# Kernel tuning notes

Hardware: AMD Instinct MI355X
Metric: run time of the kernel (lower is better)

The kernel has to match this reference:

```python
import jax, jax.numpy as jnp
import numpy as np

VOCAB, EMB, HID, OUT = 32000, 512, 1024, 8
B, S = 128, 512


def setup_inputs() -> dict:
    key = jax.random.key(0)
    ks = jax.random.split(key, 7)
    sequence_ids = jax.random.randint(ks[0], (B, S), 0, VOCAB)
    scale = 0.02
    emb = jax.random.normal(ks[1], (VOCAB, EMB), dtype=jnp.float32) * scale
    W_ih = jax.random.normal(ks[2], (4 * HID, EMB), dtype=jnp.float32) * scale
    W_hh = jax.random.normal(ks[3], (4 * HID, HID), dtype=jnp.float32) * scale
    b = jax.random.normal(ks[4], (4 * HID,), dtype=jnp.float32) * scale
    W_out = jax.random.normal(ks[5], (OUT, HID), dtype=jnp.float32) * scale
    b_out = jax.random.normal(ks[6], (OUT,), dtype=jnp.float32) * scale
    return {"sequence_ids": sequence_ids, "emb": emb, "W_ih": W_ih, "W_hh": W_hh,
            "b": b, "W_out": W_out, "b_out": b_out}


def reference(sequence_ids, emb, W_ih, W_hh, b, W_out, b_out):
    # embedding lookup: [B, S, E]
    x = emb[sequence_ids]
    Bb = x.shape[0]
    H = W_hh.shape[1]
    # precompute input projections for all timesteps at once: [S, B, 4H]
    xg = jnp.einsum('bse,ge->sbg', x, W_ih) + b

    def step(carry, xg_t):
        h, c = carry
        gates = xg_t + h @ W_hh.T  # [B, 4H]
        i, f, g, o = jnp.split(gates, 4, axis=-1)
        c = jax.nn.sigmoid(f) * c + jax.nn.sigmoid(i) * jnp.tanh(g)
        h = jax.nn.sigmoid(o) * jnp.tanh(c)
        return (h, c), None

    h0 = jnp.zeros((Bb, H), x.dtype)
    (h_last, _), _ = jax.lax.scan(step, (h0, h0), xg)
    # classifier on last hidden state: [B, OUT]
    return h_last @ W_out.T + b_out
```

## Files before the change

### kernel.cpp

```cpp
#include <hip/hip_runtime.h>
#include <cstdint>
#include <cstddef>

#define SEQ    512
#define BATCH  128
#define EMB    512
#define HID    1024
#define KTOT   1536
#define NOUT   8

#define RG     4
#define NBQ    64
#define NBLK   (RG*NBQ)
#define ROWS   32

typedef unsigned short u16;
typedef unsigned int   u32;
typedef unsigned long long u64;
typedef __attribute__((ext_vector_type(8))) __bf16 bf16x8;
typedef __attribute__((ext_vector_type(4))) float  f32x4;
typedef __attribute__((ext_vector_type(4))) float  float4v;
typedef __attribute__((ext_vector_type(4))) u16    u16x4;

#define OFF_X    0ull
#define SZ_X     ((size_t)SEQ*BATCH*EMB*2)
#define OFF_W    (OFF_X + SZ_X)
#define SZ_W     ((size_t)4*HID*KTOT*2)
#define OFF_RING (OFF_W + SZ_W)
#define SZ_RING  ((size_t)(SEQ+1)*BATCH*HID*2)
#define OFF_CNT  (OFF_RING + SZ_RING)
#define SZ_CNT   ((size_t)16*RG*64)
#define OFF_GO   (OFF_CNT + SZ_CNT)
#define SZ_GO    ((size_t)RG*64)
#define WS_NEED  (OFF_GO + SZ_GO)

__device__ inline u16 f2b(float f) {
  uint32_t u = __builtin_bit_cast(uint32_t, f);
  u = u + 0x7FFFu + ((u >> 16) & 1u);
  return (u16)(u >> 16);
}
__device__ inline float b2f(u16 u) {
  uint32_t v = ((uint32_t)u) << 16;
  return __builtin_bit_cast(float, v);
}
__device__ inline float sigm(float x) { return 1.0f / (1.0f + __expf(-x)); }
__device__ inline float tanh_(float x) {
  x = fminf(fmaxf(x, -15.f), 15.f);
  float e = __expf(2.f * x);
  return (e - 1.f) / (e + 1.f);
}
__device__ inline f32x4 mfma16(bf16x8 a, bf16x8 b, f32x4 c) {
  return __builtin_amdgcn_mfma_f32_16x16x32_bf16(a, b, c, 0, 0, 0);
}

__global__ void embed_kernel(const int* __restrict__ ids,
                             const float* __restrict__ emb,
                             u16* __restrict__ x) {
  int bid = blockIdx.x;
  int t = bid >> 7, b = bid & 127;
  int idx = ids[b * SEQ + t];
  const float4v* src = (const float4v*)(emb + (size_t)idx * EMB);
  float4v v = src[threadIdx.x];
  u16x4 o;
  o.x = f2b(v.x); o.y = f2b(v.y); o.z = f2b(v.z); o.w = f2b(v.w);
  *(u16x4*)(x + (size_t)bid * EMB + threadIdx.x * 4) = o;
}

__global__ void wpack_kernel(const float* __restrict__ Wih,
                             const float* __restrict__ Whh,
                             u16* __restrict__ Wp) {
  int gc = blockIdx.x;
  int unit = gc >> 2, q = gc & 3;
  int row = q * HID + unit;
  u16* dst = Wp + (size_t)gc * KTOT;
  for (int k = threadIdx.x; k < KTOT; k += 256) {
    float v = (k < EMB) ? Wih[(size_t)row * EMB + k]
                        : Whh[(size_t)row * HID + (k - EMB)];
    dst[k] = f2b(v);
  }
}

__global__ __launch_bounds__(256, 1) void lstm_kernel(
    const u16* __restrict__ x,
    const u16* __restrict__ Wp,
    const float* __restrict__ bias,
    u16* __restrict__ ring,
    u32* __restrict__ cnt,
    u32* __restrict__ go)
{
  __shared__ float pacc[4][ROWS][68];

  const int tid  = threadIdx.x;
  const int bid  = blockIdx.x;
  const int rg   = bid & 3;
  const int nb   = bid >> 2;
  const int lane = tid & 63;
  const int kq   = tid >> 6;
  const int l15  = lane & 15;
  const int lhi  = lane >> 4;

  const int nxc  = (kq == 0) ? 12 : (kq == 1 ? 4 : 0);
  const int arow = rg * ROWS + l15;

  bf16x8 wreg[12][4];
  {
    const int colbase = nb * 64;
    #pragma unroll
    for (int c = 0; c < 12; ++c)
      #pragma unroll
      for (int nt = 0; nt < 4; ++nt)
        wreg[c][nt] = *(const bf16x8*)(Wp
            + (size_t)(colbase + nt * 16 + l15) * KTOT
            + kq * 384 + c * 32 + lhi * 8);
  }

  const int urow = tid >> 3;
  const int up   = tid & 7;
  const int rowg = rg * ROWS + urow;
  float bs[2][4];
  #pragma unroll
  for (int k = 0; k < 2; ++k) {
    int ug = nb * 16 + 2 * up + k;
    #pragma unroll
    for (int q = 0; q < 4; ++q) bs[k][q] = bias[q * HID + ug];
  }
  float cst[2] = {0.f, 0.f};

  u32* gol = &go[rg * 16];

  bf16x8 af[2][12];
  #pragma unroll
  for (int c = 0; c < 12; ++c)
    if (c < nxc) {
      #pragma unroll
      for (int mt = 0; mt < 2; ++mt)
        af[mt][c] = *(const bf16x8*)(x + (size_t)(arow + mt * 16) * EMB
                                     + kq * 384 + c * 32 + lhi * 8);
    }

  #pragma unroll 1
  for (int t = 0; t < SEQ; ++t) {
    f32x4 acc[2][4];
    #pragma unroll
    for (int mt = 0; mt < 2; ++mt)
      #pragma unroll
      for (int nt = 0; nt < 4; ++nt) acc[mt][nt] = (f32x4){0.f, 0.f, 0.f, 0.f};
    #pragma unroll
    for (int c = 0; c < 12; ++c)
      if (c < nxc) {
        #pragma unroll
        for (int mt = 0; mt < 2; ++mt)
          #pragma unroll
          for (int nt = 0; nt < 4; ++nt)
            acc[mt][nt] = mfma16(af[mt][c], wreg[c][nt], acc[mt][nt]);
      }

    if (t > 0) {
      if (tid == 0) {
        while (__hip_atomic_load(gol, __ATOMIC_RELAXED,
                                 __HIP_MEMORY_SCOPE_AGENT) < (u32)t)
          __builtin_amdgcn_s_sleep(1);
        __asm__ __volatile__("" ::: "memory");
      }
      __syncthreads();
    }

    {
      const u16* hb = ring + (size_t)t * (BATCH * HID);
      #pragma unroll
      for (int c = 0; c < 12; ++c)
        if (c >= nxc) {
          #pragma unroll
          for (int mt = 0; mt < 2; ++mt)
            af[mt][c] = *(const bf16x8*)(hb + (size_t)(arow + mt * 16) * HID
                                         + (kq * 384 - 512 + c * 32) + lhi * 8);
        }
    }

    {
      int tn = (t + 1 < SEQ) ? (t + 1) : t;
      const u16* xb = x + (size_t)tn * (BATCH * EMB);
      #pragma unroll
      for (int c = 0; c < 12; ++c)
        if (c < nxc) {
          #pragma unroll
          for (int mt = 0; mt < 2; ++mt)
            af[mt][c] = *(const bf16x8*)(xb + (size_t)(arow + mt * 16) * EMB
                                         + kq * 384 + c * 32 + lhi * 8);
        }
    }

    #pragma unroll
    for (int c = 0; c < 12; ++c)
      if (c >= nxc) {
        #pragma unroll
        for (int mt = 0; mt < 2; ++mt)
          #pragma unroll
          for (int nt = 0; nt < 4; ++nt)
            acc[mt][nt] = mfma16(af[mt][c], wreg[c][nt], acc[mt][nt]);
      }

    #pragma unroll
    for (int mt = 0; mt < 2; ++mt)
      #pragma unroll
      for (int nt = 0; nt < 4; ++nt)
        #pragma unroll
        for (int rr = 0; rr < 4; ++rr) {
          int row = mt * 16 + lhi * 4 + rr;
          int c   = nt * 16 + l15;
          int pc  = (c & ~7) | ((c ^ row) & 7);
          pacc[kq][row][pc] = acc[mt][nt][rr];
        }
    __syncthreads();

    {
      float s[2][4];
      #pragma unroll
      for (int k = 0; k < 2; ++k)
        #pragma unroll
        for (int q = 0; q < 4; ++q) s[k][q] = bs[k][q];
      #pragma unroll
      for (int k2 = 0; k2 < 4; ++k2)
        #pragma unroll
        for (int cl = 0; cl < 8; ++cl) {
          int pc = 8 * up + ((cl ^ urow) & 7);
          s[cl >> 2][cl & 3] += pacc[k2][urow][pc];
        }
      float hv2[2];
      #pragma unroll
      for (int k = 0; k < 2; ++k) {
        float cn = sigm(s[k][1]) * cst[k] + sigm(s[k][0]) * tanh_(s[k][2]);
        cst[k] = cn;
        hv2[k] = sigm(s[k][3]) * tanh_(cn);
      }
      u32 val = (u32)f2b(hv2[0]) | ((u32)f2b(hv2[1]) << 16);
      u32* dst = (u32*)(ring + (size_t)(t + 1) * (BATCH * HID)
                        + (size_t)rowg * HID + nb * 16 + 2 * up);
      asm volatile("global_store_dword %0, %1, off sc0 sc1"
                   :: "v"(dst), "v"(val) : "memory");
    }
    asm volatile("s_waitcnt vmcnt(0)" ::: "memory");

    __syncthreads();
    if (t == SEQ - 1) break;
    if (tid == 0) {
      u32* cl_ = &cnt[((size_t)(t & 15) * RG + rg) * 16];
      u32 old = __hip_atomic_fetch_add(cl_, 1u, __ATOMIC_RELAXED,
                                       __HIP_MEMORY_SCOPE_AGENT);
      if (old == (u32)(NBQ - 1)) {
        __hip_atomic_store(cl_, 0u, __ATOMIC_RELAXED,
                           __HIP_MEMORY_SCOPE_AGENT);
        __hip_atomic_store(gol, (u32)(t + 1), __ATOMIC_RELAXED,
                           __HIP_MEMORY_SCOPE_AGENT);
      }
    }
  }
}

__global__ void head_kernel(const u16* __restrict__ h,
                            const float* __restrict__ Wout,
                            const float* __restrict__ bout,
                            float* __restrict__ out) {
  int b = blockIdx.x, l = threadIdx.x;
  float p[NOUT];
  #pragma unroll
  for (int o = 0; o < NOUT; ++o) p[o] = 0.f;
  for (int k = l; k < HID; k += 64) {
    float hv = b2f(h[(size_t)b * HID + k]);
    #pragma unroll
    for (int o = 0; o < NOUT; ++o) p[o] += hv * Wout[(size_t)o * HID + k];
  }
  #pragma unroll
  for (int o = 0; o < NOUT; ++o) {
    float v = p[o];
    #pragma unroll
    for (int off = 32; off > 0; off >>= 1) v += __shfl_down(v, off);
    if (l == 0) out[b * NOUT + o] = v + bout[o];
  }
}

__global__ void sentinel_kernel(float* out, int n) {
  int i = blockIdx.x * 256 + threadIdx.x;
  if (i < n) out[i] = 1e9f;
}

extern "C" void kernel_launch(void* const* d_in, const int* in_sizes, int n_in,
                              void* d_out, int out_size, void* d_ws, size_t ws_size,
                              hipStream_t stream) {
  const int*   ids  = (const int*)d_in[0];
  const float* emb  = (const float*)d_in[1];
  const float* Wih  = (const float*)d_in[2];
  const float* Whh  = (const float*)d_in[3];
  const float* bias = (const float*)d_in[4];
  const float* Wout = (const float*)d_in[5];
  const float* bout = (const float*)d_in[6];
  float* out = (float*)d_out;

  if (ws_size < WS_NEED) {
    sentinel_kernel<<<(out_size + 255) / 256, 256, 0, stream>>>(out, out_size);
    return;
  }

  char* ws = (char*)d_ws;
  u16* x    = (u16*)(ws + OFF_X);
  u16* Wp   = (u16*)(ws + OFF_W);
  u16* ring = (u16*)(ws + OFF_RING);
  u32* cnt  = (u32*)(ws + OFF_CNT);
  u32* go   = (u32*)(ws + OFF_GO);

  hipMemsetAsync(ring, 0, (size_t)BATCH * HID * 2, stream);
  hipMemsetAsync(cnt, 0, SZ_CNT + SZ_GO, stream);

  embed_kernel<<<SEQ * BATCH, 128, 0, stream>>>(ids, emb, x);
  wpack_kernel<<<4 * HID, 256, 0, stream>>>(Wih, Whh, Wp);

  lstm_kernel<<<NBLK, 256, 0, stream>>>(x, Wp, bias, ring, cnt, go);

  head_kernel<<<BATCH, 64, 0, stream>>>(ring + (size_t)SEQ * BATCH * HID,
                                        Wout, bout, out);
}
```

Baseline: 3.176 ms.

## Split per-row-group barrier into per-K-slice sub-barriers with per-wave waits

Replaces the single per-row-group global flag with three sub-group flags, one for each slice of hidden units that a K-quarter wave consumes. Each wave polls only the flag for its own slice, and each wave's lane 0 signals arrival, so waves can start on the slices that are ready instead of waiting for all 64 blocks. The goal is to shorten the critical path of the per-timestep global barrier. In exchange it adds more atomic traffic, drops the block-wide syncthreads around the wait, and uses a bail-out counter that could silently skip synchronization.

Result: slower. 3.302 ms (+4.0%).

```diff
diff --git a/kernel.cpp b/kernel.cpp
--- a/kernel.cpp
+++ b/kernel.cpp
@@ -13,6 +13,7 @@
 #define NBQ    64
 #define NBLK   (RG*NBQ)
 #define ROWS   32
+#define NSG    3
 
 typedef unsigned short u16;
 typedef unsigned int   u32;
@@ -29,10 +30,10 @@
 #define OFF_RING (OFF_W + SZ_W)
 #define SZ_RING  ((size_t)(SEQ+1)*BATCH*HID*2)
 #define OFF_CNT  (OFF_RING + SZ_RING)
-#define SZ_CNT   ((size_t)16*RG*64)
-#define OFF_GO   (OFF_CNT + SZ_CNT)
-#define SZ_GO    ((size_t)RG*64)
-#define WS_NEED  (OFF_GO + SZ_GO)
+#define SZ_CNT   ((size_t)16*RG*NSG*64)
+#define OFF_SGO  (OFF_CNT + SZ_CNT)
+#define SZ_SGO   ((size_t)RG*NSG*64)
+#define WS_NEED  (OFF_SGO + SZ_SGO)
 
 __device__ inline u16 f2b(float f) {
   uint32_t u = __builtin_bit_cast(uint32_t, f);
@@ -86,7 +87,7 @@
     const float* __restrict__ bias,
     u16* __restrict__ ring,
     u32* __restrict__ cnt,
-    u32* __restrict__ go)
+    u32* __restrict__ subgo)
 {
   __shared__ float pacc[4][ROWS][68];
 
@@ -102,6 +103,12 @@
   const int nxc  = (kq == 0) ? 12 : (kq == 1 ? 4 : 0);
   const int arow = rg * ROWS + l15;
 
+  const int grp  = (nb < 16) ? 0 : (nb < 40 ? 1 : 2);
+  const u32 agt  = (grp == 0) ? 64u : 96u;
+  u32* sgo_pub  = &subgo[((size_t)rg * NSG + grp) * 16];
+  const u32* sgo_mine = (kq > 0)
+      ? &subgo[((size_t)rg * NSG + (kq - 1)) * 16] : nullptr;
+
   bf16x8 wreg[12][4];
   {
     const int colbase = nb * 64;
@@ -126,8 +133,6 @@
   }
   float cst[2] = {0.f, 0.f};
 
-  u32* gol = &go[rg * 16];
-
   bf16x8 af[2][12];
   #pragma unroll
   for (int c = 0; c < 12; ++c)
@@ -155,14 +160,17 @@
             acc[mt][nt] = mfma16(af[mt][c], wreg[c][nt], acc[mt][nt]);
       }
 
-    if (t > 0) {
-      if (tid == 0) {
-        while (__hip_atomic_load(gol, __ATOMIC_RELAXED,
-                                 __HIP_MEMORY_SCOPE_AGENT) < (u32)t)
-          __builtin_amdgcn_s_sleep(1);
-        __asm__ __volatile__("" ::: "memory");
-      }
-      __syncthreads();
+    if (t > 0 && kq > 0) {
+      const u32 tgt = (u32)t;
+      int bail = 0;
+      for (;;) {
+        u32 v = __hip_atomic_load(sgo_mine, __ATOMIC_RELAXED,
+                                  __HIP_MEMORY_SCOPE_AGENT);
+        if (__all(v >= tgt)) break;
+        if (++bail > (1 << 20)) break;
+        __builtin_amdgcn_s_sleep(1);
+      }
+      __asm__ __volatile__("" ::: "memory");
     }
 
     {
@@ -213,19 +221,20 @@
         }
     __syncthreads();
 
+    float s[2][4];
+    #pragma unroll
+    for (int k = 0; k < 2; ++k)
+      #pragma unroll
+      for (int q = 0; q < 4; ++q) s[k][q] = bs[k][q];
+    #pragma unroll
+    for (int k2 = 0; k2 < 4; ++k2)
+      #pragma unroll
+      for (int cl = 0; cl < 8; ++cl) {
+        int pc = 8 * up + ((cl ^ urow) & 7);
+        s[cl >> 2][cl & 3] += pacc[k2][urow][pc];
+      }
+    __syncthreads();
     {
-      float s[2][4];
-      #pragma unroll
-      for (int k = 0; k < 2; ++k)
-        #pragma unroll
-        for (int q = 0; q < 4; ++q) s[k][q] = bs[k][q];
-      #pragma unroll
-      for (int k2 = 0; k2 < 4; ++k2)
-        #pragma unroll
-        for (int cl = 0; cl < 8; ++cl) {
-          int pc = 8 * up + ((cl ^ urow) & 7);
-          s[cl >> 2][cl & 3] += pacc[k2][urow][pc];
-        }
       float hv2[2];
       #pragma unroll
       for (int k = 0; k < 2; ++k) {
@@ -241,17 +250,17 @@
     }
     asm volatile("s_waitcnt vmcnt(0)" ::: "memory");
 
-    __syncthreads();
-    if (t == SEQ - 1) break;
-    if (tid == 0) {
-      u32* cl_ = &cnt[((size_t)(t & 15) * RG + rg) * 16];
-      u32 old = __hip_atomic_fetch_add(cl_, 1u, __ATOMIC_RELAXED,
-                                       __HIP_MEMORY_SCOPE_AGENT);
-      if (old == (u32)(NBQ - 1)) {
-        __hip_atomic_store(cl_, 0u, __ATOMIC_RELAXED,
-                           __HIP_MEMORY_SCOPE_AGENT);
-        __hip_atomic_store(gol, (u32)(t + 1), __ATOMIC_RELAXED,
-                           __HIP_MEMORY_SCOPE_AGENT);
+    if (t < SEQ - 1) {
+      if (lane == 0) {
+        u32* cl_ = &cnt[((((size_t)(t & 15) * RG) + rg) * NSG + grp) * 16];
+        u32 old = __hip_atomic_fetch_add(cl_, 1u, __ATOMIC_RELAXED,
+                                         __HIP_MEMORY_SCOPE_AGENT);
+        if (old == agt - 1u) {
+          __hip_atomic_store(cl_, 0u, __ATOMIC_RELAXED,
+                             __HIP_MEMORY_SCOPE_AGENT);
+          __hip_atomic_store(sgo_pub, (u32)(t + 1), __ATOMIC_RELAXED,
+                             __HIP_MEMORY_SCOPE_AGENT);
+        }
       }
     }
   }
@@ -302,19 +311,19 @@
   }
 
   char* ws = (char*)d_ws;
-  u16* x    = (u16*)(ws + OFF_X);
-  u16* Wp   = (u16*)(ws + OFF_W);
-  u16* ring = (u16*)(ws + OFF_RING);
-  u32* cnt  = (u32*)(ws + OFF_CNT);
-  u32* go   = (u32*)(ws + OFF_GO);
+  u16* x     = (u16*)(ws + OFF_X);
+  u16* Wp    = (u16*)(ws + OFF_W);
+  u16* ring  = (u16*)(ws + OFF_RING);
+  u32* cnt   = (u32*)(ws + OFF_CNT);
+  u32* subgo = (u32*)(ws + OFF_SGO);
 
   hipMemsetAsync(ring, 0, (size_t)BATCH * HID * 2, stream);
-  hipMemsetAsync(cnt, 0, SZ_CNT + SZ_GO, stream);
+  hipMemsetAsync(cnt, 0, SZ_CNT + SZ_SGO, stream);
 
   embed_kernel<<<SEQ * BATCH, 128, 0, stream>>>(ids, emb, x);
   wpack_kernel<<<4 * HID, 256, 0, stream>>>(Wih, Whh, Wp);
 
-  lstm_kernel<<<NBLK, 256, 0, stream>>>(x, Wp, bias, ring, cnt, go);
+  lstm_kernel<<<NBLK, 256, 0, stream>>>(x, Wp, bias, ring, cnt, subgo);
 
   head_kernel<<<BATCH, 64, 0, stream>>>(ring + (size_t)SEQ * BATCH * HID,
                                         Wout, bout, out);
```

## Replace per-group barrier counter with per-wave flags and fine-grained dependency polling

Applied to the files above, without the earlier changes.

Swaps the global atomic counter plus single go-flag barrier for per-wave progress flags. Each wave that consumes recurrent h state polls only the flags of the producer blocks whose h columns it reads, using lane-parallel loads combined with a wave vote. The x-only wave no longer waits at all. This removes the serialized atomic fetch-add, the trailing block barrier and the tid0 spin, at the cost of more polling traffic and a bail-out limit that could let a wave proceed with stale data.

After: 3.073 ms. -3.2%, faster.

```diff
diff --git a/kernel.cpp b/kernel.cpp
--- a/kernel.cpp
+++ b/kernel.cpp
@@ -28,11 +28,9 @@
 #define SZ_W     ((size_t)4*HID*KTOT*2)
 #define OFF_RING (OFF_W + SZ_W)
 #define SZ_RING  ((size_t)(SEQ+1)*BATCH*HID*2)
-#define OFF_CNT  (OFF_RING + SZ_RING)
-#define SZ_CNT   ((size_t)16*RG*64)
-#define OFF_GO   (OFF_CNT + SZ_CNT)
-#define SZ_GO    ((size_t)RG*64)
-#define WS_NEED  (OFF_GO + SZ_GO)
+#define OFF_FW   (OFF_RING + SZ_RING)
+#define SZ_FW    ((size_t)RG*NBQ*4*64)
+#define WS_NEED  (OFF_FW + SZ_FW)
 
 __device__ inline u16 f2b(float f) {
   uint32_t u = __builtin_bit_cast(uint32_t, f);
@@ -85,8 +83,7 @@
     const u16* __restrict__ Wp,
     const float* __restrict__ bias,
     u16* __restrict__ ring,
-    u32* __restrict__ cnt,
-    u32* __restrict__ go)
+    u32* __restrict__ fw)
 {
   __shared__ float pacc[4][ROWS][68];
 
@@ -102,6 +99,15 @@
   const int nxc  = (kq == 0) ? 12 : (kq == 1 ? 4 : 0);
   const int arow = rg * ROWS + l15;
 
+  u32* fw_own = &fw[(((size_t)rg * NBQ + nb) * 4 + kq) * 16];
+  const int pbase = (kq == 1) ? 0 : (kq == 2 ? 16 : 40);
+  const int nflag = (kq == 1) ? 64 : 96;
+  const u32* fp0 = &fw[(((size_t)rg * NBQ + pbase + (lane >> 2)) * 4 + (lane & 3)) * 16];
+  const int  f2i = lane + 64;
+  const u32* fp1 = (f2i < nflag)
+      ? &fw[(((size_t)rg * NBQ + pbase + (f2i >> 2)) * 4 + (f2i & 3)) * 16]
+      : fp0;
+
   bf16x8 wreg[12][4];
   {
     const int colbase = nb * 64;
@@ -126,8 +132,6 @@
   }
   float cst[2] = {0.f, 0.f};
 
-  u32* gol = &go[rg * 16];
-
   bf16x8 af[2][12];
   #pragma unroll
   for (int c = 0; c < 12; ++c)
@@ -155,14 +159,17 @@
             acc[mt][nt] = mfma16(af[mt][c], wreg[c][nt], acc[mt][nt]);
       }
 
-    if (t > 0) {
-      if (tid == 0) {
-        while (__hip_atomic_load(gol, __ATOMIC_RELAXED,
-                                 __HIP_MEMORY_SCOPE_AGENT) < (u32)t)
-          __builtin_amdgcn_s_sleep(1);
-        __asm__ __volatile__("" ::: "memory");
-      }
-      __syncthreads();
+    if (t > 0 && kq > 0) {
+      const u32 tgt = (u32)t;
+      int bail = 0;
+      for (;;) {
+        u32 a = __hip_atomic_load(fp0, __ATOMIC_RELAXED, __HIP_MEMORY_SCOPE_AGENT);
+        u32 b = __hip_atomic_load(fp1, __ATOMIC_RELAXED, __HIP_MEMORY_SCOPE_AGENT);
+        if (__all((a >= tgt) & (b >= tgt))) break;
+        if (++bail > (1 << 20)) break;
+        __builtin_amdgcn_s_sleep(1);
+      }
+      __asm__ __volatile__("" ::: "memory");
     }
 
     {
@@ -213,19 +220,21 @@
         }
     __syncthreads();
 
+    float s[2][4];
+    #pragma unroll
+    for (int k = 0; k < 2; ++k)
+      #pragma unroll
+      for (int q = 0; q < 4; ++q) s[k][q] = bs[k][q];
+    #pragma unroll
+    for (int k2 = 0; k2 < 4; ++k2)
+      #pragma unroll
+      for (int cl = 0; cl < 8; ++cl) {
+        int pc = 8 * up + ((cl ^ urow) & 7);
+        s[cl >> 2][cl & 3] += pacc[k2][urow][pc];
+      }
+    __syncthreads();
+
     {
-      float s[2][4];
-      #pragma unroll
-      for (int k = 0; k < 2; ++k)
-        #pragma unroll
-        for (int q = 0; q < 4; ++q) s[k][q] = bs[k][q];
-      #pragma unroll
-      for (int k2 = 0; k2 < 4; ++k2)
-        #pragma unroll
-        for (int cl = 0; cl < 8; ++cl) {
-          int pc = 8 * up + ((cl ^ urow) & 7);
-          s[cl >> 2][cl & 3] += pacc[k2][urow][pc];
-        }
       float hv2[2];
       #pragma unroll
       for (int k = 0; k < 2; ++k) {
@@ -241,18 +250,9 @@
     }
     asm volatile("s_waitcnt vmcnt(0)" ::: "memory");
 
-    __syncthreads();
-    if (t == SEQ - 1) break;
-    if (tid == 0) {
-      u32* cl_ = &cnt[((size_t)(t & 15) * RG + rg) * 16];
-      u32 old = __hip_atomic_fetch_add(cl_, 1u, __ATOMIC_RELAXED,
-                                       __HIP_MEMORY_SCOPE_AGENT);
-      if (old == (u32)(NBQ - 1)) {
-        __hip_atomic_store(cl_, 0u, __ATOMIC_RELAXED,
-                           __HIP_MEMORY_SCOPE_AGENT);
-        __hip_atomic_store(gol, (u32)(t + 1), __ATOMIC_RELAXED,
-                           __HIP_MEMORY_SCOPE_AGENT);
-      }
+    if (t < SEQ - 1 && lane == 0) {
+      __hip_atomic_store(fw_own, (u32)(t + 1), __ATOMIC_RELAXED,
+                         __HIP_MEMORY_SCOPE_AGENT);
     }
   }
 }
@@ -305,16 +305,15 @@
   u16* x    = (u16*)(ws + OFF_X);
   u16* Wp   = (u16*)(ws + OFF_W);
   u16* ring = (u16*)(ws + OFF_RING);
-  u32* cnt  = (u32*)(ws + OFF_CNT);
-  u32* go   = (u32*)(ws + OFF_GO);
+  u32* fwv  = (u32*)(ws + OFF_FW);
 
   hipMemsetAsync(ring, 0, (size_t)BATCH * HID * 2, stream);
-  hipMemsetAsync(cnt, 0, SZ_CNT + SZ_GO, stream);
+  hipMemsetAsync(fwv, 0, SZ_FW, stream);
 
   embed_kernel<<<SEQ * BATCH, 128, 0, stream>>>(ids, emb, x);
   wpack_kernel<<<4 * HID, 256, 0, stream>>>(Wih, Whh, Wp);
 
-  lstm_kernel<<<NBLK, 256, 0, stream>>>(x, Wp, bias, ring, cnt, go);
+  lstm_kernel<<<NBLK, 256, 0, stream>>>(x, Wp, bias, ring, fwv);
 
   head_kernel<<<BATCH, 64, 0, stream>>>(ring + (size_t)SEQ * BATCH * HID,
                                         Wout, bout, out);
```

## Repartition LSTM into 8 batch pods with per-block flags and XCC-local sync

Applied to the files above, without the earlier changes.

Repartitions the persistent LSTM grid into 8 batch pods of 16 rows by 32 column blocks, each holding 128 gate columns. 96 columns live in registers and 32 in LDS. The central counter-plus-go barrier is replaced by per-block progress flags that 32 lanes poll in parallel. Each block records its XCC ID at startup, and when all blocks in a pod share one XCC it uses non-coherent-scope stores and loads to cut cross-die cache traffic. The risks are extra LDS weight reads inside the inner MFMA loop, and a correctness dependence on how the hardware places blocks onto XCCs.

Result: slower. 3.392 ms (+6.8%).

```diff
diff --git a/kernel.cpp b/kernel.cpp
--- a/kernel.cpp
+++ b/kernel.cpp
@@ -9,14 +9,16 @@
 #define KTOT   1536
 #define NOUT   8
 
-#define RG     4
-#define NBQ    64
-#define NBLK   (RG*NBQ)
-#define ROWS   32
+#define NPOD   8
+#define NCB    32
+#define NBLK   (NPOD*NCB)
+#define ROWS   16
+#define WLSTR  1544
+
+#define GETREG_XCC 63508
 
 typedef unsigned short u16;
 typedef unsigned int   u32;
-typedef unsigned long long u64;
 typedef __attribute__((ext_vector_type(8))) __bf16 bf16x8;
 typedef __attribute__((ext_vector_type(4))) float  f32x4;
 typedef __attribute__((ext_vector_type(4))) float  float4v;
@@ -28,11 +30,15 @@
 #define SZ_W     ((size_t)4*HID*KTOT*2)
 #define OFF_RING (OFF_W + SZ_W)
 #define SZ_RING  ((size_t)(SEQ+1)*BATCH*HID*2)
-#define OFF_CNT  (OFF_RING + SZ_RING)
-#define SZ_CNT   ((size_t)16*RG*64)
-#define OFF_GO   (OFF_CNT + SZ_CNT)
-#define SZ_GO    ((size_t)RG*64)
-#define WS_NEED  (OFF_GO + SZ_GO)
+#define OFF_FW   (OFF_RING + SZ_RING)
+#define SZ_FW    ((size_t)NBLK*64)
+#define OFF_XT   (OFF_FW + SZ_FW)
+#define SZ_XT    (4096ull)
+#define WS_NEED  (OFF_XT + SZ_XT)
+
+#define SMEM_W   ((size_t)32*WLSTR*2)
+#define SMEM_P   ((size_t)4*ROWS*136*4)
+#define SMEM_BYTES (SMEM_W + SMEM_P)
 
 __device__ inline u16 f2b(float f) {
   uint32_t u = __builtin_bit_cast(uint32_t, f);
@@ -85,81 +91,129 @@
     const u16* __restrict__ Wp,
     const float* __restrict__ bias,
     u16* __restrict__ ring,
-    u32* __restrict__ cnt,
-    u32* __restrict__ go)
+    u32* __restrict__ fw,
+    u32* __restrict__ xtab)
 {
-  __shared__ float pacc[4][ROWS][68];
+  extern __shared__ char smem[];
+  u16*   wl   = (u16*)smem;
+  float* pacc = (float*)(smem + SMEM_W);
+  __shared__ int smode;
 
   const int tid  = threadIdx.x;
   const int bid  = blockIdx.x;
-  const int rg   = bid & 3;
-  const int nb   = bid >> 2;
+  const int pod  = bid & 7;
+  const int cb   = bid >> 3;
   const int lane = tid & 63;
   const int kq   = tid >> 6;
   const int l15  = lane & 15;
   const int lhi  = lane >> 4;
 
   const int nxc  = (kq == 0) ? 12 : (kq == 1 ? 4 : 0);
-  const int arow = rg * ROWS + l15;
-
-  bf16x8 wreg[12][4];
+  const int arow = pod * ROWS + l15;
+
+  const u32 myx = (__builtin_amdgcn_s_getreg(GETREG_XCC) & 0xFu) | 0x10u;
+  if (tid == 0) {
+    smode = 0;
+    __hip_atomic_store(&xtab[bid], myx, __ATOMIC_RELAXED,
+                       __HIP_MEMORY_SCOPE_AGENT);
+  }
+
+  bf16x8 wreg[12][6];
   {
-    const int colbase = nb * 64;
+    const int colbase = cb * 128;
     #pragma unroll
     for (int c = 0; c < 12; ++c)
       #pragma unroll
-      for (int nt = 0; nt < 4; ++nt)
+      for (int nt = 0; nt < 6; ++nt)
         wreg[c][nt] = *(const bf16x8*)(Wp
             + (size_t)(colbase + nt * 16 + l15) * KTOT
             + kq * 384 + c * 32 + lhi * 8);
   }
-
-  const int urow = tid >> 3;
-  const int up   = tid & 7;
-  const int rowg = rg * ROWS + urow;
+  for (int e = tid * 8; e < 32 * KTOT; e += 256 * 8) {
+    int col = e / KTOT;
+    int k   = e - col * KTOT;
+    *(bf16x8*)&wl[col * WLSTR + k] =
+        *(const bf16x8*)(Wp + (size_t)(cb * 128 + 96 + col) * KTOT + k);
+  }
+
+  __syncthreads();
+  if (tid < 64) {
+    const int peer = 8 * (lane & 31) + pod;
+    u32 xv = 0; int bail = 0;
+    for (;;) {
+      xv = __hip_atomic_load(&xtab[peer], __ATOMIC_RELAXED,
+                             __HIP_MEMORY_SCOPE_AGENT);
+      if (xv != 0) break;
+      if (++bail > (1 << 18)) break;
+      __builtin_amdgcn_s_sleep(1);
+    }
+    int ok = __all(xv == myx) ? 1 : 0;
+    if (lane == 0) smode = ok;
+  }
+  __syncthreads();
+  const int fast = smode;
+
+  const int urow = tid >> 4;
+  const int u    = tid & 15;
   float bs[2][4];
   #pragma unroll
   for (int k = 0; k < 2; ++k) {
-    int ug = nb * 16 + 2 * up + k;
+    int ug = cb * 32 + u + k * 16;
     #pragma unroll
     for (int q = 0; q < 4; ++q) bs[k][q] = bias[q * HID + ug];
   }
   float cst[2] = {0.f, 0.f};
 
-  u32* gol = &go[rg * 16];
-
-  bf16x8 af[2][12];
+  const u16* wlb  = &wl[l15 * WLSTR + kq * 384 + lhi * 8];
+  u32* fw_own = &fw[(size_t)bid * 16];
+
+  bf16x8 af[12];
   #pragma unroll
   for (int c = 0; c < 12; ++c)
-    if (c < nxc) {
-      #pragma unroll
-      for (int mt = 0; mt < 2; ++mt)
-        af[mt][c] = *(const bf16x8*)(x + (size_t)(arow + mt * 16) * EMB
-                                     + kq * 384 + c * 32 + lhi * 8);
-    }
+    if (c < nxc)
+      af[c] = *(const bf16x8*)(x + (size_t)arow * EMB + kq * 384 + c * 32 + lhi * 8);
 
   #pragma unroll 1
   for (int t = 0; t < SEQ; ++t) {
-    f32x4 acc[2][4];
-    #pragma unroll
-    for (int mt = 0; mt < 2; ++mt)
-      #pragma unroll
-      for (int nt = 0; nt < 4; ++nt) acc[mt][nt] = (f32x4){0.f, 0.f, 0.f, 0.f};
+    f32x4 acc[8];
+    #pragma unroll
+    for (int nt = 0; nt < 8; ++nt) acc[nt] = (f32x4){0.f, 0.f, 0.f, 0.f};
     #pragma unroll
     for (int c = 0; c < 12; ++c)
       if (c < nxc) {
         #pragma unroll
-        for (int mt = 0; mt < 2; ++mt)
-          #pragma unroll
-          for (int nt = 0; nt < 4; ++nt)
-            acc[mt][nt] = mfma16(af[mt][c], wreg[c][nt], acc[mt][nt]);
+        for (int nt = 0; nt < 6; ++nt)
+          acc[nt] = mfma16(af[c], wreg[c][nt], acc[nt]);
+        bf16x8 w6 = *(const bf16x8*)(wlb + c * 32);
+        bf16x8 w7 = *(const bf16x8*)(wlb + 16 * WLSTR + c * 32);
+        acc[6] = mfma16(af[c], w6, acc[6]);
+        acc[7] = mfma16(af[c], w7, acc[7]);
       }
 
     if (t > 0) {
-      if (tid == 0) {
-        while (__hip_atomic_load(gol, __ATOMIC_RELAXED,
-                                 __HIP_MEMORY_SCOPE_AGENT) < (u32)t)
-          __builtin_amdgcn_s_sleep(1);
+      if (tid < 64) {
+        const u32 tgt = (u32)t;
+        const u32* fp = &fw[(size_t)(8 * (lane & 31) + pod) * 16];
+        int bail = 0;
+        if (fast) {
+          for (;;) {
+            u32 v;
+            asm volatile("global_load_dword %0, %1, off sc0\n\t"
+                         "s_waitcnt vmcnt(0)"
+                         : "=v"(v) : "v"(fp) : "memory");
+            if (__all(v >= tgt)) break;
+            if (++bail > (1 << 18)) break;
+            __builtin_amdgcn_s_sleep(1);
+          }
+        } else {
+          for (;;) {
+            u32 v = __hip_atomic_load(fp, __ATOMIC_RELAXED,
+                                      __HIP_MEMORY_SCOPE_AGENT);
+            if (__all(v >= tgt)) break;
+            if (++bail > (1 << 18)) break;
+            __builtin_amdgcn_s_sleep(1);
+          }
+        }
         __asm__ __volatile__("" ::: "memory");
       }
       __syncthreads();
@@ -169,12 +223,9 @@
       const u16* hb = ring + (size_t)t * (BATCH * HID);
       #pragma unroll
       for (int c = 0; c < 12; ++c)
-        if (c >= nxc) {
-          #pragma unroll
-          for (int mt = 0; mt < 2; ++mt)
-            af[mt][c] = *(const bf16x8*)(hb + (size_t)(arow + mt * 16) * HID
-                                         + (kq * 384 - 512 + c * 32) + lhi * 8);
-        }
+        if (c >= nxc)
+          af[c] = *(const bf16x8*)(hb + (size_t)arow * HID
+                                   + (kq * 384 - 512 + c * 32) + lhi * 8);
     }
 
     {
@@ -182,50 +233,52 @@
       const u16* xb = x + (size_t)tn * (BATCH * EMB);
       #pragma unroll
       for (int c = 0; c < 12; ++c)
-        if (c < nxc) {
-          #pragma unroll
-          for (int mt = 0; mt < 2; ++mt)
-            af[mt][c] = *(const bf16x8*)(xb + (size_t)(arow + mt * 16) * EMB
-                                         + kq * 384 + c * 32 + lhi * 8);
-        }
+        if (c < nxc)
+          af[c] = *(const bf16x8*)(xb + (size_t)arow * EMB
+                                   + kq * 384 + c * 32 + lhi * 8);
     }
 
     #pragma unroll
     for (int c = 0; c < 12; ++c)
       if (c >= nxc) {
         #pragma unroll
-        for (int mt = 0; mt < 2; ++mt)
-          #pragma unroll
-          for (int nt = 0; nt < 4; ++nt)
-            acc[mt][nt] = mfma16(af[mt][c], wreg[c][nt], acc[mt][nt]);
-      }
-
-    #pragma unroll
-    for (int mt = 0; mt < 2; ++mt)
-      #pragma unroll
-      for (int nt = 0; nt < 4; ++nt)
+        for (int nt = 0; nt < 6; ++nt)
+          acc[nt] = mfma16(af[c], wreg[c][nt], acc[nt]);
+        bf16x8 w6 = *(const bf16x8*)(wlb + c * 32);
+        bf16x8 w7 = *(const bf16x8*)(wlb + 16 * WLSTR + c * 32);
+        acc[6] = mfma16(af[c], w6, acc[6]);
+        acc[7] = mfma16(af[c], w7, acc[7]);
+      }
+
+    #pragma unroll
+    for (int nt = 0; nt < 8; ++nt)
+      #pragma unroll
+      for (int rr = 0; rr < 4; ++rr) {
+        int row = lhi * 4 + rr;
+        int c   = nt * 16 + l15;
+        int pc  = (c & ~7) | ((c ^ row) & 7);
+        pacc[(kq * ROWS + row) * 136 + pc] = acc[nt][rr];
+      }
+    __syncthreads();
+
+    float s[2][4];
+    #pragma unroll
+    for (int k = 0; k < 2; ++k)
+      #pragma unroll
+      for (int q = 0; q < 4; ++q) s[k][q] = bs[k][q];
+    #pragma unroll
+    for (int k2 = 0; k2 < 4; ++k2)
+      #pragma unroll
+      for (int k = 0; k < 2; ++k)
         #pragma unroll
-        for (int rr = 0; rr < 4; ++rr) {
-          int row = mt * 16 + lhi * 4 + rr;
-          int c   = nt * 16 + l15;
-          int pc  = (c & ~7) | ((c ^ row) & 7);
-          pacc[kq][row][pc] = acc[mt][nt][rr];
+        for (int q = 0; q < 4; ++q) {
+          int c  = (u + k * 16) * 4 + q;
+          int pc = (c & ~7) | ((c ^ urow) & 7);
+          s[k][q] += pacc[(k2 * ROWS + urow) * 136 + pc];
         }
     __syncthreads();
 
     {
-      float s[2][4];
-      #pragma unroll
-      for (int k = 0; k < 2; ++k)
-        #pragma unroll
-        for (int q = 0; q < 4; ++q) s[k][q] = bs[k][q];
-      #pragma unroll
-      for (int k2 = 0; k2 < 4; ++k2)
-        #pragma unroll
-        for (int cl = 0; cl < 8; ++cl) {
-          int pc = 8 * up + ((cl ^ urow) & 7);
-          s[cl >> 2][cl & 3] += pacc[k2][urow][pc];
-        }
       float hv2[2];
       #pragma unroll
       for (int k = 0; k < 2; ++k) {
@@ -233,24 +286,37 @@
         cst[k] = cn;
         hv2[k] = sigm(s[k][3]) * tanh_(cn);
       }
-      u32 val = (u32)f2b(hv2[0]) | ((u32)f2b(hv2[1]) << 16);
-      u32* dst = (u32*)(ring + (size_t)(t + 1) * (BATCH * HID)
-                        + (size_t)rowg * HID + nb * 16 + 2 * up);
-      asm volatile("global_store_dword %0, %1, off sc0 sc1"
-                   :: "v"(dst), "v"(val) : "memory");
+      float o0 = __shfl_xor(hv2[0], 1);
+      float o1 = __shfl_xor(hv2[1], 1);
+      if ((u & 1) == 0) {
+        u16* hw = ring + (size_t)(t + 1) * (BATCH * HID)
+                  + (size_t)(pod * ROWS + urow) * HID + cb * 32;
+        u32 v0 = (u32)f2b(hv2[0]) | ((u32)f2b(o0) << 16);
+        u32 v1 = (u32)f2b(hv2[1]) | ((u32)f2b(o1) << 16);
+        u32* d0 = (u32*)&hw[u];
+        u32* d1 = (u32*)&hw[u + 16];
+        if (fast) {
+          asm volatile("global_store_dword %0, %2, off\n\t"
+                       "global_store_dword %1, %3, off"
+                       :: "v"(d0), "v"(d1), "v"(v0), "v"(v1) : "memory");
+        } else {
+          asm volatile("global_store_dword %0, %2, off sc0 sc1\n\t"
+                       "global_store_dword %1, %3, off sc0 sc1"
+                       :: "v"(d0), "v"(d1), "v"(v0), "v"(v1) : "memory");
+        }
+      }
     }
     asm volatile("s_waitcnt vmcnt(0)" ::: "memory");
 
     __syncthreads();
     if (t == SEQ - 1) break;
     if (tid == 0) {
-      u32* cl_ = &cnt[((size_t)(t & 15) * RG + rg) * 16];
-      u32 old = __hip_atomic_fetch_add(cl_, 1u, __ATOMIC_RELAXED,
-                                       __HIP_MEMORY_SCOPE_AGENT);
-      if (old == (u32)(NBQ - 1)) {
-        __hip_atomic_store(cl_, 0u, __ATOMIC_RELAXED,
-                           __HIP_MEMORY_SCOPE_AGENT);
-        __hip_atomic_store(gol, (u32)(t + 1), __ATOMIC_RELAXED,
+      u32 v = (u32)(t + 1);
+      if (fast) {
+        asm volatile("global_store_dword %0, %1, off sc0"
+                     :: "v"(fw_own), "v"(v) : "memory");
+      } else {
+        __hip_atomic_store(fw_own, v, __ATOMIC_RELAXED,
                            __HIP_MEMORY_SCOPE_AGENT);
       }
     }
@@ -305,16 +371,19 @@
   u16* x    = (u16*)(ws + OFF_X);
   u16* Wp   = (u16*)(ws + OFF_W);
   u16* ring = (u16*)(ws + OFF_RING);
-  u32* cnt  = (u32*)(ws + OFF_CNT);
-  u32* go   = (u32*)(ws + OFF_GO);
+  u32* fwv  = (u32*)(ws + OFF_FW);
+  u32* xtab = (u32*)(ws + OFF_XT);
 
   hipMemsetAsync(ring, 0, (size_t)BATCH * HID * 2, stream);
-  hipMemsetAsync(cnt, 0, SZ_CNT + SZ_GO, stream);
+  hipMemsetAsync(fwv, 0, SZ_FW + SZ_XT, stream);
 
   embed_kernel<<<SEQ * BATCH, 128, 0, stream>>>(ids, emb, x);
   wpack_kernel<<<4 * HID, 256, 0, stream>>>(Wih, Whh, Wp);
 
-  lstm_kernel<<<NBLK, 256, 0, stream>>>(x, Wp, bias, ring, cnt, go);
+  hipFuncSetAttribute((const void*)lstm_kernel,
+                      hipFuncAttributeMaxDynamicSharedMemorySize,
+                      (int)SMEM_BYTES);
+  lstm_kernel<<<NBLK, 256, SMEM_BYTES, stream>>>(x, Wp, bias, ring, fwv, xtab);
 
   head_kernel<<<BATCH, 64, 0, stream>>>(ring + (size_t)SEQ * BATCH * HID,
                                         Wout, bout, out);
```
